# Optimization experiments

Measured on AMD Instinct MI355X. Metric: run time of the kernel, lower is better.

## Reference

```python
import jax, jax.numpy as jnp
import numpy as np

E, H, I, T = 8, 1024, 2816, 512
E4M3_MAX = 448.0  # torch.finfo(float8_e4m3fn).max


def _quantize_to_fp8(w):
    # per-tensor dynamic scaling, identical to quantize_to_fp8 in the source
    amax = jnp.max(jnp.abs(w))
    scale = jnp.maximum(amax / E4M3_MAX, 1e-12)
    fp8 = (w / scale).astype(jnp.float8_e4m3fn)
    return fp8, scale.reshape(1).astype(jnp.float32)


def setup_inputs() -> dict:
    key = jax.random.key(0)
    k1, k2, k3, k4 = jax.random.split(key, 4)
    x = jax.random.normal(k1, (T, H), jnp.float32)
    expert_idx = jax.random.randint(k2, (T,), 0, E)
    # learned 3D expert params (stored compressed as fp8 + per-tensor scale)
    w_gu = jax.random.normal(k3, (E, 2 * I, H), jnp.float32) * 0.02
    w_d = jax.random.normal(k4, (E, H, I), jnp.float32) * 0.02
    w_gu_fp8, w_gu_scale = _quantize_to_fp8(w_gu)
    w_d_fp8, w_d_scale = _quantize_to_fp8(w_d)
    return {
        "x": x,
        "expert_idx": expert_idx,
        "w_gu_fp8": w_gu_fp8,
        "w_gu_scale": w_gu_scale,
        "w_d_fp8": w_d_fp8,
        "w_d_scale": w_d_scale,
    }


def reference(x, expert_idx, w_gu_fp8, w_gu_scale, w_d_fp8, w_d_scale):
    # materialize(): dequantize fp8 -> high precision (fp8.to(dtype) * scale)
    w_gu = w_gu_fp8.astype(jnp.float32) * w_gu_scale  # [E, 2I, H]
    w_d = w_d_fp8.astype(jnp.float32) * w_d_scale     # [E, H, I]
    # inner experts forward: SwiGLU MLP per expert, top-1 routed tokens
    gu = jnp.einsum('th,efh->tef', x, w_gu)            # [T, E, 2I]
    gate, up = jnp.split(gu, 2, axis=-1)               # [T, E, I] each
    h = jax.nn.silu(gate) * up                          # [T, E, I]
    y = jnp.einsum('tei,ehi->teh', h, w_d)              # [T, E, H]
    out = y[jnp.arange(x.shape[0]), expert_idx]         # [T, H] select routed expert
    return out
```

## Files before the change

### kernel.cpp

```cpp
#include <hip/hip_runtime.h>
#include <hip/hip_bf16.h>
#include <stdint.h>

#define E_ 8
#define H_ 1024
#define I_ 2816
#define T_ 512

typedef __attribute__((ext_vector_type(4))) float f32x4;
typedef __attribute__((ext_vector_type(8))) short short8;

typedef __attribute__((address_space(1))) const unsigned GAS;
typedef __attribute__((address_space(3))) unsigned LAS;

__device__ __forceinline__ void dma16(const void* g, void* l) {
    __builtin_amdgcn_global_load_lds((GAS*)g, (LAS*)l, 16, 0, 0);
}
__device__ __forceinline__ unsigned short f2bf(float f) {
    return __builtin_bit_cast(unsigned short, __float2bfloat16(f));
}
__device__ __forceinline__ uint32_t pack_rne(float lo, float hi) {
    return (uint32_t)f2bf(lo) | ((uint32_t)f2bf(hi) << 16);
}
__device__ __forceinline__ uint32_t pack_trunc(float lo, float hi) {
    return (__builtin_bit_cast(uint32_t, hi) & 0xFFFF0000u) |
           (__builtin_bit_cast(uint32_t, lo) >> 16);
}

#define VM6() asm volatile("s_waitcnt vmcnt(6)" ::: "memory")
#define VM0() asm volatile("s_waitcnt vmcnt(0)" ::: "memory")

__global__ __launch_bounds__(256) void route_cvt(const float* __restrict__ x,
                                                 const int* __restrict__ idx,
                                                 int* __restrict__ counts,
                                                 int* __restrict__ bucket,
                                                 unsigned short* __restrict__ xg) {
    int tid = threadIdx.x;
    if (blockIdx.x == 0) {
        if (tid < E_) counts[tid] = 0;
        for (int i = tid; i < E_ * T_; i += 256) bucket[i] = 0;
        __syncthreads();
#pragma unroll
        for (int k = 0; k < 2; ++k) {
            int t = tid + k * 256;
            int e = idx[t];
            int pos = atomicAdd(counts + e, 1);
            bucket[e * T_ + pos] = t;
        }
    }
    int unit = blockIdx.x * 256 + tid;
    const float* xp = x + (size_t)unit * 8;
    float4 a = *(const float4*)xp, b = *(const float4*)(xp + 4);
    uint4 o = make_uint4(pack_rne(a.x, a.y), pack_rne(a.z, a.w),
                         pack_rne(b.x, b.y), pack_rne(b.z, b.w));
    *(uint4*)(xg + (size_t)unit * 8) = o;
}

__global__ __launch_bounds__(256) void gemm1(const unsigned short* __restrict__ xg,
                                             const float* __restrict__ wgu,
                                             const float* __restrict__ sgu_p,
                                             const int* __restrict__ counts,
                                             const int* __restrict__ bucket,
                                             __hip_bfloat16* __restrict__ hbuf) {
    int e = blockIdx.x >> 1, mt = blockIdx.x & 1;
    int cnt = counts[e];
    if (mt * 64 >= cnt) return;
    int f0 = blockIdx.y * 32;

    __shared__ __align__(16) char smem[72 * 1024 + 256];
    int* tok = (int*)(smem + 72 * 1024);
    int tid = threadIdx.x, w = tid >> 6, lane = tid & 63;
    int r16 = lane & 15, kg = lane >> 4;

    float sgu = sgu_p[0];
    asm volatile("" :: "v"(sgu));

    if (tid < 64) tok[tid] = bucket[e * T_ + mt * 64 + tid];
    __syncthreads();

    const char* xb = (const char*)xg;
    const char* srcA[2]; char* dstA[2];
#pragma unroll
    for (int i = 0; i < 2; ++i) {
        int U = (w * 2 + i) * 64 + lane;
        int row = U >> 3, sl = U & 7;
        srcA[i] = xb + (size_t)tok[row] * 2048 + (size_t)((sl ^ (row & 7)) * 16);
        dstA[i] = smem + (w * 2 + i) * 1024;
    }
    const char* wg_e = (const char*)(wgu + (size_t)e * 2 * (size_t)I_ * H_);
    const char* srcB[4]; char* dstB[4];
#pragma unroll
    for (int i = 0; i < 4; ++i) {
        int U = (w * 4 + i) * 64 + lane;
        int row = U >> 4, sl = U & 15;
        int wr = (row < 32) ? (f0 + row) : (I_ + f0 + row - 32);
        srcB[i] = wg_e + (size_t)wr * 4096 + (size_t)((sl ^ (row & 15)) * 16);
        dstB[i] = smem + 24 * 1024 + (w * 4 + i) * 1024;
    }

#define G1_ISSUE(s, buf)                                                     \
    do {                                                                     \
        _Pragma("unroll")                                                    \
        for (int i = 0; i < 2; ++i) dma16(srcA[i] + (size_t)(s) * 128, dstA[i] + (buf) * 8192);  \
        _Pragma("unroll")                                                    \
        for (int i = 0; i < 4; ++i) dma16(srcB[i] + (size_t)(s) * 256, dstB[i] + (buf) * 16384); \
    } while (0)

    G1_ISSUE(0, 0);
    G1_ISSUE(1, 1);

    f32x4 acc[4];
#pragma unroll
    for (int m = 0; m < 4; ++m) acc[m] = (f32x4){0, 0, 0, 0};

    for (int t = 0; t < 16; ++t) {
        VM6();
        __builtin_amdgcn_s_barrier();
        int tp = (t + 2 < 16) ? t + 2 : 15;
        G1_ISSUE(tp, (t + 2) % 3);
        const char* Ab = smem + (t % 3) * 8192;
        const char* Bb = smem + 24 * 1024 + (t % 3) * 16384;
#pragma unroll
        for (int kk = 0; kk < 2; ++kk) {
            int brow = w * 16 + r16;
            int bo = brow * 256 + kk * 128 + kg * 32;
            int sw = r16 << 4;
            float4 b0 = *(float4*)(Bb + (bo ^ sw));
            float4 b1 = *(float4*)(Bb + ((bo + 16) ^ sw));
            uint4 bu = make_uint4(pack_trunc(b0.x, b0.y), pack_trunc(b0.z, b0.w),
                                  pack_trunc(b1.x, b1.y), pack_trunc(b1.z, b1.w));
            short8 B = __builtin_bit_cast(short8, bu);
#pragma unroll
            for (int m = 0; m < 4; ++m) {
                int ar = m * 16 + r16;
                short8 A = *(short8*)(Ab + ((ar * 128 + kk * 64 + kg * 16) ^ ((ar & 7) << 4)));
                acc[m] = __builtin_amdgcn_mfma_f32_16x16x32_bf16(A, B, acc[m], 0, 0, 0);
            }
        }
    }
    VM0();
    __syncthreads();

    float* ex = (float*)smem;
    if (w >= 2) {
        float* dst = ex + (w - 2) * 1024;
#pragma unroll
        for (int m = 0; m < 4; ++m)
#pragma unroll
            for (int j = 0; j < 4; ++j)
                dst[(m * 16 + kg * 4 + j) * 16 + r16] = acc[m][j] * sgu;
    }
    __syncthreads();
    if (w < 2) {
        const float* src = ex + w * 1024;
#pragma unroll
        for (int m = 0; m < 4; ++m)
#pragma unroll
            for (int j = 0; j < 4; ++j) {
                int tr = m * 16 + kg * 4 + j;
                int pos = mt * 64 + tr;
                if (pos < cnt) {
                    float g = acc[m][j] * sgu;
                    float u = src[tr * 16 + r16];
                    float hv = (g / (1.f + __expf(-g))) * u;
                    hbuf[(size_t)tok[tr] * I_ + f0 + w * 16 + r16] = __float2bfloat16(hv);
                }
            }
    }
}

__global__ __launch_bounds__(256) void gemm2(const __hip_bfloat16* __restrict__ hbuf,
                                             const float* __restrict__ wd,
                                             const float* __restrict__ sd_p,
                                             const int* __restrict__ counts,
                                             const int* __restrict__ bucket,
                                             float* __restrict__ out) {
    int e = blockIdx.x >> 1, mt = blockIdx.x & 1;
    int cnt = counts[e];
    if (mt * 64 >= cnt) return;
    int h0 = blockIdx.y * 16;

    __shared__ __align__(16) char smem[72 * 1024 + 256];
    int* tok = (int*)(smem + 72 * 1024);
    int tid = threadIdx.x, w = tid >> 6, lane = tid & 63;
    int r16 = lane & 15, kg = lane >> 4;

    float sd = sd_p[0];
    asm volatile("" :: "v"(sd));

    if (tid < 64) tok[tid] = bucket[e * T_ + mt * 64 + tid];
    __syncthreads();

    const char* hb = (const char*)hbuf;
    const char* srcA[4]; char* dstA[4];
#pragma unroll
    for (int i = 0; i < 4; ++i) {
        int U = (w * 4 + i) * 64 + lane;
        int row = U >> 4, sl = U & 15;
        srcA[i] = hb + (size_t)tok[row] * (I_ * 2) + (size_t)((sl ^ (row & 15)) * 16);
        dstA[i] = smem + (w * 4 + i) * 1024;
    }
    const char* wd_e = (const char*)(wd + (size_t)e * (size_t)H_ * I_);
    const char* srcB[2]; char* dstB[2];
#pragma unroll
    for (int i = 0; i < 2; ++i) {
        int U = (w * 2 + i) * 64 + lane;
        int row = U >> 5, sl = U & 31;
        srcB[i] = wd_e + (size_t)(h0 + row) * ((size_t)I_ * 4) + (size_t)((sl ^ (row & 15)) * 16);
        dstB[i] = smem + 48 * 1024 + (w * 2 + i) * 1024;
    }

#define G2_ISSUE(s, buf)                                                     \
    do {                                                                     \
        _Pragma("unroll")                                                    \
        for (int i = 0; i < 4; ++i) dma16(srcA[i] + (size_t)(s) * 256, dstA[i] + (buf) * 16384); \
        _Pragma("unroll")                                                    \
        for (int i = 0; i < 2; ++i) dma16(srcB[i] + (size_t)(s) * 512, dstB[i] + (buf) * 8192);  \
    } while (0)

    G2_ISSUE(0, 0);
    G2_ISSUE(1, 1);

    f32x4 acc = (f32x4){0, 0, 0, 0};

    for (int t = 0; t < 22; ++t) {
        VM6();
        __builtin_amdgcn_s_barrier();
        int tp = (t + 2 < 22) ? t + 2 : 21;
        G2_ISSUE(tp, (t + 2) % 3);
        const char* Ab = smem + (t % 3) * 16384;
        const char* Bb = smem + 48 * 1024 + (t % 3) * 8192;
#pragma unroll
        for (int kk = 0; kk < 4; ++kk) {
            int bo = r16 * 512 + kk * 128 + kg * 32;
            int sw = r16 << 4;
            float4 b0 = *(float4*)(Bb + (bo ^ sw));
            float4 b1 = *(float4*)(Bb + ((bo + 16) ^ sw));
            uint4 bu = make_uint4(pack_trunc(b0.x, b0.y), pack_trunc(b0.z, b0.w),
                                  pack_trunc(b1.x, b1.y), pack_trunc(b1.z, b1.w));
            short8 B = __builtin_bit_cast(short8, bu);
            int ar = w * 16 + r16;
            short8 A = *(short8*)(Ab + ((ar * 256 + kk * 64 + kg * 16) ^ ((ar & 15) << 4)));
            acc = __builtin_amdgcn_mfma_f32_16x16x32_bf16(A, B, acc, 0, 0, 0);
        }
    }
    VM0();

#pragma unroll
    for (int j = 0; j < 4; ++j) {
        int tr = w * 16 + kg * 4 + j;
        int pos = mt * 64 + tr;
        if (pos < cnt)
            out[(size_t)tok[tr] * H_ + h0 + r16] = acc[j] * sd;
    }
}

extern "C" void kernel_launch(void* const* d_in, const int* in_sizes, int n_in,
                              void* d_out, int out_size, void* d_ws, size_t ws_size,
                              hipStream_t stream) {
    const float* x    = (const float*)d_in[0];
    const int*   eidx = (const int*)d_in[1];
    const float* wgu  = (const float*)d_in[2];
    const float* sgu  = (const float*)d_in[3];
    const float* wd   = (const float*)d_in[4];
    const float* sd   = (const float*)d_in[5];
    float* out = (float*)d_out;

    char* ws = (char*)d_ws;
    int* counts = (int*)ws;
    int* bucket = (int*)(ws + 1024);
    unsigned short* xg = (unsigned short*)(ws + 32768);
    __hip_bfloat16* hbuf = (__hip_bfloat16*)(ws + 1114112);

    route_cvt<<<256, 256, 0, stream>>>(x, eidx, counts, bucket, xg);
    gemm1<<<dim3(E_ * 2, I_ / 32), 256, 0, stream>>>(xg, wgu, sgu, counts, bucket, hbuf);
    gemm2<<<dim3(E_ * 2, H_ / 16), 256, 0, stream>>>(hbuf, wd, sd, counts, bucket, out);
}
```

Measured before the change: 121.7 us.

## Widen token tile to 128 rows so each expert's weights stream once

Both GEMMs now cover up to 128 routed tokens per block instead of 64. The per-step K slice is halved, so the three-stage LDS pipeline still fits and the loop runs more iterations. With about 64 tokens per expert on average, the old tiling made experts with more than 64 tokens read their fp32 weight slices twice, and the larger tile is meant to remove that duplicate traffic. gemm2 also doubles its output width to 32 columns using a 2x2 warp layout. The cost is wasted MFMA work on padded rows and more accumulator registers per thread.

After: 238.8 us. 1.96x slower.

```diff
diff --git a/kernel.cpp b/kernel.cpp
--- a/kernel.cpp
+++ b/kernel.cpp
@@ -28,6 +28,7 @@
 }
 
 #define VM6() asm volatile("s_waitcnt vmcnt(6)" ::: "memory")
+#define VM4() asm volatile("s_waitcnt vmcnt(4)" ::: "memory")
 #define VM0() asm volatile("s_waitcnt vmcnt(0)" ::: "memory")
 
 __global__ __launch_bounds__(256) void route_cvt(const float* __restrict__ x,
@@ -62,103 +63,92 @@
                                              const int* __restrict__ counts,
                                              const int* __restrict__ bucket,
                                              __hip_bfloat16* __restrict__ hbuf) {
-    int e = blockIdx.x >> 1, mt = blockIdx.x & 1;
+    int e = blockIdx.x >> 2, mt = blockIdx.x & 3;
     int cnt = counts[e];
-    if (mt * 64 >= cnt) return;
+    if (mt * 128 >= cnt) return;
     int f0 = blockIdx.y * 32;
 
-    __shared__ __align__(16) char smem[72 * 1024 + 256];
-    int* tok = (int*)(smem + 72 * 1024);
+    __shared__ __align__(16) char smem[48 * 1024 + 512];
+    int* tok = (int*)(smem + 48 * 1024);
     int tid = threadIdx.x, w = tid >> 6, lane = tid & 63;
     int r16 = lane & 15, kg = lane >> 4;
 
-    float sgu = sgu_p[0];
-    asm volatile("" :: "v"(sgu));
-
-    if (tid < 64) tok[tid] = bucket[e * T_ + mt * 64 + tid];
+    if (tid < 128) tok[tid] = bucket[e * T_ + mt * 128 + tid];
     __syncthreads();
 
     const char* xb = (const char*)xg;
     const char* srcA[2]; char* dstA[2];
 #pragma unroll
     for (int i = 0; i < 2; ++i) {
-        int U = (w * 2 + i) * 64 + lane;
-        int row = U >> 3, sl = U & 7;
-        srcA[i] = xb + (size_t)tok[row] * 2048 + (size_t)((sl ^ (row & 7)) * 16);
-        dstA[i] = smem + (w * 2 + i) * 1024;
-    }
-    const char* wg_e = (const char*)(wgu + (size_t)e * 2 * (size_t)I_ * H_);
-    const char* srcB[4]; char* dstB[4];
-#pragma unroll
-    for (int i = 0; i < 4; ++i) {
-        int U = (w * 4 + i) * 64 + lane;
-        int row = U >> 4, sl = U & 15;
+        int gi = w * 2 + i;
+        int row = gi * 16 + (lane >> 2), sl = lane & 3;
+        srcA[i] = xb + (size_t)tok[row] * 2048 + sl * 16;
+        dstA[i] = smem + gi * 1024;
+    }
+    const char* wg_e = (const char*)wgu + (size_t)e * (2 * (size_t)I_ * H_ * 4);
+    const char* srcB[2]; char* dstB[2];
+#pragma unroll
+    for (int i = 0; i < 2; ++i) {
+        int gi = w * 2 + i;
+        int row = gi * 8 + (lane >> 3), sl = lane & 7;
         int wr = (row < 32) ? (f0 + row) : (I_ + f0 + row - 32);
-        srcB[i] = wg_e + (size_t)wr * 4096 + (size_t)((sl ^ (row & 15)) * 16);
-        dstB[i] = smem + 24 * 1024 + (w * 4 + i) * 1024;
-    }
-
-#define G1_ISSUE(s, buf)                                                     \
-    do {                                                                     \
-        _Pragma("unroll")                                                    \
-        for (int i = 0; i < 2; ++i) dma16(srcA[i] + (size_t)(s) * 128, dstA[i] + (buf) * 8192);  \
-        _Pragma("unroll")                                                    \
-        for (int i = 0; i < 4; ++i) dma16(srcB[i] + (size_t)(s) * 256, dstB[i] + (buf) * 16384); \
-    } while (0)
-
-    G1_ISSUE(0, 0);
-    G1_ISSUE(1, 1);
-
-    f32x4 acc[4];
-#pragma unroll
-    for (int m = 0; m < 4; ++m) acc[m] = (f32x4){0, 0, 0, 0};
-
-    for (int t = 0; t < 16; ++t) {
-        VM6();
+        srcB[i] = wg_e + (size_t)wr * 4096 + ((sl ^ (row & 7)) * 16);
+        dstB[i] = smem + 24 * 1024 + gi * 1024;
+    }
+
+#define G1I(s, b) do {                                                               \
+    _Pragma("unroll")                                                                \
+    for (int i = 0; i < 2; ++i) dma16(srcA[i] + (size_t)(s) * 64,  dstA[i] + (b) * 8192); \
+    _Pragma("unroll")                                                                \
+    for (int i = 0; i < 2; ++i) dma16(srcB[i] + (size_t)(s) * 128, dstB[i] + (b) * 8192); } while (0)
+
+    G1I(0, 0);
+    G1I(1, 1);
+
+    f32x4 acc[8];
+#pragma unroll
+    for (int m = 0; m < 8; ++m) acc[m] = (f32x4){0, 0, 0, 0};
+
+    for (int t = 0; t < 32; ++t) {
+        if (t < 30) { VM4(); } else { VM0(); }
+        __builtin_amdgcn_sched_barrier(0);
         __builtin_amdgcn_s_barrier();
-        int tp = (t + 2 < 16) ? t + 2 : 15;
-        G1_ISSUE(tp, (t + 2) % 3);
+        if (t + 2 < 32) G1I(t + 2, (t + 2) % 3);
         const char* Ab = smem + (t % 3) * 8192;
-        const char* Bb = smem + 24 * 1024 + (t % 3) * 16384;
-#pragma unroll
-        for (int kk = 0; kk < 2; ++kk) {
-            int brow = w * 16 + r16;
-            int bo = brow * 256 + kk * 128 + kg * 32;
-            int sw = r16 << 4;
-            float4 b0 = *(float4*)(Bb + (bo ^ sw));
-            float4 b1 = *(float4*)(Bb + ((bo + 16) ^ sw));
-            uint4 bu = make_uint4(pack_trunc(b0.x, b0.y), pack_trunc(b0.z, b0.w),
-                                  pack_trunc(b1.x, b1.y), pack_trunc(b1.z, b1.w));
-            short8 B = __builtin_bit_cast(short8, bu);
-#pragma unroll
-            for (int m = 0; m < 4; ++m) {
-                int ar = m * 16 + r16;
-                short8 A = *(short8*)(Ab + ((ar * 128 + kk * 64 + kg * 16) ^ ((ar & 7) << 4)));
-                acc[m] = __builtin_amdgcn_mfma_f32_16x16x32_bf16(A, B, acc[m], 0, 0, 0);
-            }
-        }
-    }
-    VM0();
-    __syncthreads();
-
+        const char* Bb = smem + 24 * 1024 + (t % 3) * 8192;
+        int br = w * 16 + r16;
+        float4 b0 = *(const float4*)(Bb + br * 128 + (((2 * kg)     ^ (br & 7)) * 16));
+        float4 b1 = *(const float4*)(Bb + br * 128 + (((2 * kg + 1) ^ (br & 7)) * 16));
+        uint4 bu = make_uint4(pack_trunc(b0.x, b0.y), pack_trunc(b0.z, b0.w),
+                              pack_trunc(b1.x, b1.y), pack_trunc(b1.z, b1.w));
+        short8 B = __builtin_bit_cast(short8, bu);
+#pragma unroll
+        for (int m = 0; m < 8; ++m) {
+            short8 A = *(const short8*)(Ab + (m * 16 + r16) * 64 + kg * 16);
+            acc[m] = __builtin_amdgcn_mfma_f32_16x16x32_bf16(A, B, acc[m], 0, 0, 0);
+        }
+    }
+    __syncthreads();
+
+    float sgu = sgu_p[0];
     float* ex = (float*)smem;
     if (w >= 2) {
-        float* dst = ex + (w - 2) * 1024;
-#pragma unroll
-        for (int m = 0; m < 4; ++m)
+        float* dst = ex + (w - 2) * 2048;
+#pragma unroll
+        for (int m = 0; m < 8; ++m)
 #pragma unroll
             for (int j = 0; j < 4; ++j)
                 dst[(m * 16 + kg * 4 + j) * 16 + r16] = acc[m][j] * sgu;
     }
     __syncthreads();
     if (w < 2) {
-        const float* src = ex + w * 1024;
-#pragma unroll
-        for (int m = 0; m < 4; ++m)
+        const float* src = ex + w * 2048;
+#pragma unroll
+        for (int m = 0; m < 8; ++m)
 #pragma unroll
             for (int j = 0; j < 4; ++j) {
                 int tr = m * 16 + kg * 4 + j;
-                int pos = mt * 64 + tr;
+                int pos = mt * 128 + tr;
                 if (pos < cnt) {
                     float g = acc[m][j] * sgu;
                     float u = src[tr * 16 + r16];
@@ -175,84 +165,86 @@
                                              const int* __restrict__ counts,
                                              const int* __restrict__ bucket,
                                              float* __restrict__ out) {
-    int e = blockIdx.x >> 1, mt = blockIdx.x & 1;
+    int e = blockIdx.x >> 2, mt = blockIdx.x & 3;
     int cnt = counts[e];
-    if (mt * 64 >= cnt) return;
-    int h0 = blockIdx.y * 16;
-
-    __shared__ __align__(16) char smem[72 * 1024 + 256];
+    if (mt * 128 >= cnt) return;
+    int h0 = blockIdx.y * 32;
+
+    __shared__ __align__(16) char smem[72 * 1024 + 512];
     int* tok = (int*)(smem + 72 * 1024);
     int tid = threadIdx.x, w = tid >> 6, lane = tid & 63;
     int r16 = lane & 15, kg = lane >> 4;
-
-    float sd = sd_p[0];
-    asm volatile("" :: "v"(sd));
-
-    if (tid < 64) tok[tid] = bucket[e * T_ + mt * 64 + tid];
+    int mg = w >> 1, ng = w & 1;
+
+    if (tid < 128) tok[tid] = bucket[e * T_ + mt * 128 + tid];
     __syncthreads();
 
     const char* hb = (const char*)hbuf;
     const char* srcA[4]; char* dstA[4];
 #pragma unroll
     for (int i = 0; i < 4; ++i) {
-        int U = (w * 4 + i) * 64 + lane;
-        int row = U >> 4, sl = U & 15;
-        srcA[i] = hb + (size_t)tok[row] * (I_ * 2) + (size_t)((sl ^ (row & 15)) * 16);
-        dstA[i] = smem + (w * 4 + i) * 1024;
-    }
-    const char* wd_e = (const char*)(wd + (size_t)e * (size_t)H_ * I_);
+        int gi = w * 4 + i;
+        int row = gi * 8 + (lane >> 3), sl = lane & 7;
+        srcA[i] = hb + (size_t)tok[row] * 5632 + ((sl ^ (row & 7)) * 16);
+        dstA[i] = smem + gi * 1024;
+    }
+    const char* wd_e = (const char*)wd + (size_t)e * ((size_t)H_ * I_ * 4);
     const char* srcB[2]; char* dstB[2];
 #pragma unroll
     for (int i = 0; i < 2; ++i) {
-        int U = (w * 2 + i) * 64 + lane;
-        int row = U >> 5, sl = U & 31;
-        srcB[i] = wd_e + (size_t)(h0 + row) * ((size_t)I_ * 4) + (size_t)((sl ^ (row & 15)) * 16);
-        dstB[i] = smem + 48 * 1024 + (w * 2 + i) * 1024;
-    }
-
-#define G2_ISSUE(s, buf)                                                     \
-    do {                                                                     \
-        _Pragma("unroll")                                                    \
-        for (int i = 0; i < 4; ++i) dma16(srcA[i] + (size_t)(s) * 256, dstA[i] + (buf) * 16384); \
-        _Pragma("unroll")                                                    \
-        for (int i = 0; i < 2; ++i) dma16(srcB[i] + (size_t)(s) * 512, dstB[i] + (buf) * 8192);  \
-    } while (0)
-
-    G2_ISSUE(0, 0);
-    G2_ISSUE(1, 1);
-
-    f32x4 acc = (f32x4){0, 0, 0, 0};
-
-    for (int t = 0; t < 22; ++t) {
-        VM6();
+        int gi = w * 2 + i;
+        int row = gi * 4 + (lane >> 4), sl = lane & 15;
+        srcB[i] = wd_e + (size_t)(h0 + row) * 11264 + ((sl ^ (row & 15)) * 16);
+        dstB[i] = smem + 48 * 1024 + gi * 1024;
+    }
+
+#define G2I(s, b) do {                                                                \
+    _Pragma("unroll")                                                                 \
+    for (int i = 0; i < 4; ++i) dma16(srcA[i] + (size_t)(s) * 128, dstA[i] + (b) * 16384); \
+    _Pragma("unroll")                                                                 \
+    for (int i = 0; i < 2; ++i) dma16(srcB[i] + (size_t)(s) * 256, dstB[i] + (b) * 8192);  } while (0)
+
+    G2I(0, 0);
+    G2I(1, 1);
+
+    f32x4 acc[4];
+#pragma unroll
+    for (int m = 0; m < 4; ++m) acc[m] = (f32x4){0, 0, 0, 0};
+
+    for (int t = 0; t < 44; ++t) {
+        if (t < 42) { VM6(); } else { VM0(); }
+        __builtin_amdgcn_sched_barrier(0);
         __builtin_amdgcn_s_barrier();
-        int tp = (t + 2 < 22) ? t + 2 : 21;
-        G2_ISSUE(tp, (t + 2) % 3);
+        if (t + 2 < 44) G2I(t + 2, (t + 2) % 3);
         const char* Ab = smem + (t % 3) * 16384;
         const char* Bb = smem + 48 * 1024 + (t % 3) * 8192;
 #pragma unroll
-        for (int kk = 0; kk < 4; ++kk) {
-            int bo = r16 * 512 + kk * 128 + kg * 32;
-            int sw = r16 << 4;
-            float4 b0 = *(float4*)(Bb + (bo ^ sw));
-            float4 b1 = *(float4*)(Bb + ((bo + 16) ^ sw));
+        for (int kk = 0; kk < 2; ++kk) {
+            int brow = ng * 16 + r16;
+            float4 b0 = *(const float4*)(Bb + brow * 256 + (((kk * 8 + 2 * kg)     ^ (brow & 15)) * 16));
+            float4 b1 = *(const float4*)(Bb + brow * 256 + (((kk * 8 + 2 * kg + 1) ^ (brow & 15)) * 16));
             uint4 bu = make_uint4(pack_trunc(b0.x, b0.y), pack_trunc(b0.z, b0.w),
                                   pack_trunc(b1.x, b1.y), pack_trunc(b1.z, b1.w));
             short8 B = __builtin_bit_cast(short8, bu);
-            int ar = w * 16 + r16;
-            short8 A = *(short8*)(Ab + ((ar * 256 + kk * 64 + kg * 16) ^ ((ar & 15) << 4)));
-            acc = __builtin_amdgcn_mfma_f32_16x16x32_bf16(A, B, acc, 0, 0, 0);
-        }
-    }
-    VM0();
-
-#pragma unroll
-    for (int j = 0; j < 4; ++j) {
-        int tr = w * 16 + kg * 4 + j;
-        int pos = mt * 64 + tr;
-        if (pos < cnt)
-            out[(size_t)tok[tr] * H_ + h0 + r16] = acc[j] * sd;
-    }
+#pragma unroll
+            for (int m = 0; m < 4; ++m) {
+                int arow = mg * 64 + m * 16 + r16;
+                short8 A = *(const short8*)(Ab + arow * 128 + (((kk * 4 + kg) ^ (arow & 7)) * 16));
+                acc[m] = __builtin_amdgcn_mfma_f32_16x16x32_bf16(A, B, acc[m], 0, 0, 0);
+            }
+        }
+    }
+
+    float sd = sd_p[0];
+#pragma unroll
+    for (int m = 0; m < 4; ++m)
+#pragma unroll
+        for (int j = 0; j < 4; ++j) {
+            int tr = mg * 64 + m * 16 + kg * 4 + j;
+            int pos = mt * 128 + tr;
+            if (pos < cnt)
+                out[(size_t)tok[tr] * H_ + h0 + ng * 16 + r16] = acc[m][j] * sd;
+        }
 }
 
 extern "C" void kernel_launch(void* const* d_in, const int* in_sizes, int n_in,
@@ -273,6 +265,6 @@
     __hip_bfloat16* hbuf = (__hip_bfloat16*)(ws + 1114112);
 
     route_cvt<<<256, 256, 0, stream>>>(x, eidx, counts, bucket, xg);
-    gemm1<<<dim3(E_ * 2, I_ / 32), 256, 0, stream>>>(xg, wgu, sgu, counts, bucket, hbuf);
-    gemm2<<<dim3(E_ * 2, H_ / 16), 256, 0, stream>>>(hbuf, wd, sd, counts, bucket, out);
-}
+    gemm1<<<dim3(E_ * 4, I_ / 32), 256, 0, stream>>>(xg, wgu, sgu, counts, bucket, hbuf);
+    gemm2<<<dim3(E_ * 4, H_ / 32), 256, 0, stream>>>(hbuf, wd, sd, counts, bucket, out);
+}
```

## Restructure gemm1 to stream weights from registers with 128-token tiles

Applied to the files above, without the earlier changes.

gemm1 now handles all 128 token slots of an expert per block (one M tile instead of two) and 64 feature columns, so each weight row is read once per expert rather than twice. Weights are loaded directly into registers with a two-deep software prefetch instead of DMA into LDS. Activations are gathered into LDS in four K-chunks. Gate and up accumulators live in the same wave, which removes the LDS exchange in the SwiGLU epilogue. The risks are the hard assumption of at most 128 tokens per expert, higher register pressure from 16 accumulators, and extra barriers around each activation reload.

After: 116.2 us. -4.5%, faster.

```diff
diff --git a/kernel.cpp b/kernel.cpp
--- a/kernel.cpp
+++ b/kernel.cpp
@@ -62,111 +62,95 @@
                                              const int* __restrict__ counts,
                                              const int* __restrict__ bucket,
                                              __hip_bfloat16* __restrict__ hbuf) {
-    int e = blockIdx.x >> 1, mt = blockIdx.x & 1;
+    int e = blockIdx.x;
     int cnt = counts[e];
-    if (mt * 64 >= cnt) return;
-    int f0 = blockIdx.y * 32;
-
-    __shared__ __align__(16) char smem[72 * 1024 + 256];
-    int* tok = (int*)(smem + 72 * 1024);
+    int f0 = blockIdx.y * 64;
+
+    __shared__ __align__(16) char sA[64 * 1024 + 512];
+    int* tok = (int*)(sA + 64 * 1024);
     int tid = threadIdx.x, w = tid >> 6, lane = tid & 63;
     int r16 = lane & 15, kg = lane >> 4;
 
+    const float* gp = wgu + (size_t)e * 2 * (size_t)I_ * H_ +
+                      (size_t)(f0 + w * 16 + r16) * H_ + kg * 8;
+    const float* up = gp + (size_t)I_ * H_;
+
+#define LOADW(NX, GA, GB, UA, UB)                                   \
+    do {                                                            \
+        const float* p_ = gp + (size_t)(NX) * 32;                   \
+        GA = *(const float4*)p_; GB = *(const float4*)(p_ + 4);     \
+        const float* q_ = up + (size_t)(NX) * 32;                   \
+        UA = *(const float4*)q_; UB = *(const float4*)(q_ + 4);     \
+    } while (0)
+
+    float4 g0a, g0b, u0a, u0b, g1a, g1b, u1a, u1b;
+    LOADW(0, g0a, g0b, u0a, u0b);
+    LOADW(1, g1a, g1b, u1a, u1b);
+
+    if (tid < 128) tok[tid] = bucket[e * T_ + tid];
+    __syncthreads();
+
+    f32x4 accg[8], accu[8];
+#pragma unroll
+    for (int m = 0; m < 8; ++m) { accg[m] = (f32x4){0,0,0,0}; accu[m] = (f32x4){0,0,0,0}; }
+
+#define CSTEP(J, GA, GB, UA, UB)                                                        \
+    do {                                                                                \
+        uint4 bg_ = make_uint4(pack_trunc((GA).x,(GA).y), pack_trunc((GA).z,(GA).w),    \
+                               pack_trunc((GB).x,(GB).y), pack_trunc((GB).z,(GB).w));   \
+        uint4 bu_ = make_uint4(pack_trunc((UA).x,(UA).y), pack_trunc((UA).z,(UA).w),    \
+                               pack_trunc((UB).x,(UB).y), pack_trunc((UB).z,(UB).w));   \
+        short8 Bg_ = __builtin_bit_cast(short8, bg_);                                   \
+        short8 Bu_ = __builtin_bit_cast(short8, bu_);                                   \
+        const char* ab_ = sA + (((J) * 4 + kg) << 11);                                  \
+        _Pragma("unroll")                                                               \
+        for (int m_ = 0; m_ < 8; ++m_) {                                                \
+            short8 A_ = *(const short8*)(ab_ + ((m_ * 16 + r16) << 4));                 \
+            accg[m_] = __builtin_amdgcn_mfma_f32_16x16x32_bf16(A_, Bg_, accg[m_],0,0,0);\
+            accu[m_] = __builtin_amdgcn_mfma_f32_16x16x32_bf16(A_, Bu_, accu[m_],0,0,0);\
+        }                                                                               \
+    } while (0)
+
+    for (int q = 0; q < 4; ++q) {
+        __syncthreads();
+#pragma unroll
+        for (int i = 0; i < 16; ++i) {
+            int u = tid + i * 256;
+            int s = u >> 7, t_ = u & 127;
+            uint4 v = *(const uint4*)(xg + (size_t)tok[t_] * H_ + q * 256 + s * 8);
+            *(uint4*)(sA + s * 2048 + t_ * 16) = v;
+        }
+        __syncthreads();
+#pragma unroll
+        for (int j = 0; j < 8; j += 2) {
+            CSTEP(j, g0a, g0b, u0a, u0b);
+            {
+                int nx = q * 8 + j + 2; if (nx > 31) nx = 31;
+                LOADW(nx, g0a, g0b, u0a, u0b);
+            }
+            CSTEP(j + 1, g1a, g1b, u1a, u1b);
+            {
+                int nx = q * 8 + j + 3; if (nx > 31) nx = 31;
+                LOADW(nx, g1a, g1b, u1a, u1b);
+            }
+        }
+    }
+
     float sgu = sgu_p[0];
-    asm volatile("" :: "v"(sgu));
-
-    if (tid < 64) tok[tid] = bucket[e * T_ + mt * 64 + tid];
-    __syncthreads();
-
-    const char* xb = (const char*)xg;
-    const char* srcA[2]; char* dstA[2];
-#pragma unroll
-    for (int i = 0; i < 2; ++i) {
-        int U = (w * 2 + i) * 64 + lane;
-        int row = U >> 3, sl = U & 7;
-        srcA[i] = xb + (size_t)tok[row] * 2048 + (size_t)((sl ^ (row & 7)) * 16);
-        dstA[i] = smem + (w * 2 + i) * 1024;
-    }
-    const char* wg_e = (const char*)(wgu + (size_t)e * 2 * (size_t)I_ * H_);
-    const char* srcB[4]; char* dstB[4];
-#pragma unroll
-    for (int i = 0; i < 4; ++i) {
-        int U = (w * 4 + i) * 64 + lane;
-        int row = U >> 4, sl = U & 15;
-        int wr = (row < 32) ? (f0 + row) : (I_ + f0 + row - 32);
-        srcB[i] = wg_e + (size_t)wr * 4096 + (size_t)((sl ^ (row & 15)) * 16);
-        dstB[i] = smem + 24 * 1024 + (w * 4 + i) * 1024;
-    }
-
-#define G1_ISSUE(s, buf)                                                     \
-    do {                                                                     \
-        _Pragma("unroll")                                                    \
-        for (int i = 0; i < 2; ++i) dma16(srcA[i] + (size_t)(s) * 128, dstA[i] + (buf) * 8192);  \
-        _Pragma("unroll")                                                    \
-        for (int i = 0; i < 4; ++i) dma16(srcB[i] + (size_t)(s) * 256, dstB[i] + (buf) * 16384); \
-    } while (0)
-
-    G1_ISSUE(0, 0);
-    G1_ISSUE(1, 1);
-
-    f32x4 acc[4];
-#pragma unroll
-    for (int m = 0; m < 4; ++m) acc[m] = (f32x4){0, 0, 0, 0};
-
-    for (int t = 0; t < 16; ++t) {
-        VM6();
-        __builtin_amdgcn_s_barrier();
-        int tp = (t + 2 < 16) ? t + 2 : 15;
-        G1_ISSUE(tp, (t + 2) % 3);
-        const char* Ab = smem + (t % 3) * 8192;
-        const char* Bb = smem + 24 * 1024 + (t % 3) * 16384;
-#pragma unroll
-        for (int kk = 0; kk < 2; ++kk) {
-            int brow = w * 16 + r16;
-            int bo = brow * 256 + kk * 128 + kg * 32;
-            int sw = r16 << 4;
-            float4 b0 = *(float4*)(Bb + (bo ^ sw));
-            float4 b1 = *(float4*)(Bb + ((bo + 16) ^ sw));
-            uint4 bu = make_uint4(pack_trunc(b0.x, b0.y), pack_trunc(b0.z, b0.w),
-                                  pack_trunc(b1.x, b1.y), pack_trunc(b1.z, b1.w));
-            short8 B = __builtin_bit_cast(short8, bu);
-#pragma unroll
-            for (int m = 0; m < 4; ++m) {
-                int ar = m * 16 + r16;
-                short8 A = *(short8*)(Ab + ((ar * 128 + kk * 64 + kg * 16) ^ ((ar & 7) << 4)));
-                acc[m] = __builtin_amdgcn_mfma_f32_16x16x32_bf16(A, B, acc[m], 0, 0, 0);
+#pragma unroll
+    for (int m = 0; m < 8; ++m)
+#pragma unroll
+        for (int j = 0; j < 4; ++j) {
+            int tr = m * 16 + kg * 4 + j;
+            if (tr < cnt) {
+                float g = accg[m][j] * sgu;
+                float u = accu[m][j] * sgu;
+                float hv = (g / (1.f + __expf(-g))) * u;
+                hbuf[(size_t)tok[tr] * I_ + f0 + w * 16 + r16] = __float2bfloat16(hv);
             }
         }
-    }
-    VM0();
-    __syncthreads();
-
-    float* ex = (float*)smem;
-    if (w >= 2) {
-        float* dst = ex + (w - 2) * 1024;
-#pragma unroll
-        for (int m = 0; m < 4; ++m)
-#pragma unroll
-            for (int j = 0; j < 4; ++j)
-                dst[(m * 16 + kg * 4 + j) * 16 + r16] = acc[m][j] * sgu;
-    }
-    __syncthreads();
-    if (w < 2) {
-        const float* src = ex + w * 1024;
-#pragma unroll
-        for (int m = 0; m < 4; ++m)
-#pragma unroll
-            for (int j = 0; j < 4; ++j) {
-                int tr = m * 16 + kg * 4 + j;
-                int pos = mt * 64 + tr;
-                if (pos < cnt) {
-                    float g = acc[m][j] * sgu;
-                    float u = src[tr * 16 + r16];
-                    float hv = (g / (1.f + __expf(-g))) * u;
-                    hbuf[(size_t)tok[tr] * I_ + f0 + w * 16 + r16] = __float2bfloat16(hv);
-                }
-            }
-    }
+#undef CSTEP
+#undef LOADW
 }
 
 __global__ __launch_bounds__(256) void gemm2(const __hip_bfloat16* __restrict__ hbuf,
@@ -253,6 +237,7 @@
         if (pos < cnt)
             out[(size_t)tok[tr] * H_ + h0 + r16] = acc[j] * sd;
     }
+#undef G2_ISSUE
 }
 
 extern "C" void kernel_launch(void* const* d_in, const int* in_sizes, int n_in,
@@ -273,6 +258,6 @@
     __hip_bfloat16* hbuf = (__hip_bfloat16*)(ws + 1114112);
 
     route_cvt<<<256, 256, 0, stream>>>(x, eidx, counts, bucket, xg);
-    gemm1<<<dim3(E_ * 2, I_ / 32), 256, 0, stream>>>(xg, wgu, sgu, counts, bucket, hbuf);
+    gemm1<<<dim3(E_, I_ / 64), 256, 0, stream>>>(xg, wgu, sgu, counts, bucket, hbuf);
     gemm2<<<dim3(E_ * 2, H_ / 16), 256, 0, stream>>>(hbuf, wd, sd, counts, bucket, out);
 }
```

## Restructure gemm1 to one block per expert with fused gate/up accumulators

Applied to the files above, without the earlier changes.

gemm1 now covers all of an expert's tokens (up to 128) in a single block over a narrower 16-feature slice. Each gate/up weight tile is therefore streamed from memory once per expert, not once per 64-token M tile. Each warp keeps separate gate and up accumulators, so the LDS exchange and the extra barriers in the SwiGLU epilogue go away. The pipeline is reworked to double-buffer activations and triple-buffer weights. The cost is more activation traffic per block and wasted MFMA work on empty token rows. It also assumes no expert receives more than 128 tokens.

Result: faster. 113.8 us (-6.5%).

```diff
diff --git a/kernel.cpp b/kernel.cpp
--- a/kernel.cpp
+++ b/kernel.cpp
@@ -27,6 +27,7 @@
            (__builtin_bit_cast(uint32_t, lo) >> 16);
 }
 
+#define VM2() asm volatile("s_waitcnt vmcnt(2)" ::: "memory")
 #define VM6() asm volatile("s_waitcnt vmcnt(6)" ::: "memory")
 #define VM0() asm volatile("s_waitcnt vmcnt(0)" ::: "memory")
 
@@ -62,111 +63,100 @@
                                              const int* __restrict__ counts,
                                              const int* __restrict__ bucket,
                                              __hip_bfloat16* __restrict__ hbuf) {
-    int e = blockIdx.x >> 1, mt = blockIdx.x & 1;
+    int e = blockIdx.x;
+    int f0 = blockIdx.y * 16;
     int cnt = counts[e];
-    if (mt * 64 >= cnt) return;
-    int f0 = blockIdx.y * 32;
-
-    __shared__ __align__(16) char smem[72 * 1024 + 256];
-    int* tok = (int*)(smem + 72 * 1024);
+
+    __shared__ __align__(16) char smem[56 * 1024 + 512];
+    int* tok = (int*)(smem + 56 * 1024);
     int tid = threadIdx.x, w = tid >> 6, lane = tid & 63;
     int r16 = lane & 15, kg = lane >> 4;
 
-    float sgu = sgu_p[0];
-    asm volatile("" :: "v"(sgu));
-
-    if (tid < 64) tok[tid] = bucket[e * T_ + mt * 64 + tid];
+    if (tid < 128) tok[tid] = bucket[e * T_ + tid];
     __syncthreads();
 
     const char* xb = (const char*)xg;
-    const char* srcA[2]; char* dstA[2];
+    const char* srcA[4]; char* dstA[4];
+#pragma unroll
+    for (int i = 0; i < 4; ++i) {
+        int U = (w * 4 + i) * 64 + lane;
+        int t_ = U >> 3, sl = U & 7;
+        srcA[i] = xb + (size_t)tok[t_] * 2048 + ((sl ^ (t_ & 7)) * 16);
+        dstA[i] = smem + (w * 4 + i) * 1024;
+    }
+    const char* wbase = (const char*)wgu + (size_t)e * 2 * (size_t)I_ * H_ * 4;
+    const char* srcB[2]; char* dstB[2];
 #pragma unroll
     for (int i = 0; i < 2; ++i) {
         int U = (w * 2 + i) * 64 + lane;
-        int row = U >> 3, sl = U & 7;
-        srcA[i] = xb + (size_t)tok[row] * 2048 + (size_t)((sl ^ (row & 7)) * 16);
-        dstA[i] = smem + (w * 2 + i) * 1024;
-    }
-    const char* wg_e = (const char*)(wgu + (size_t)e * 2 * (size_t)I_ * H_);
-    const char* srcB[4]; char* dstB[4];
-#pragma unroll
-    for (int i = 0; i < 4; ++i) {
-        int U = (w * 4 + i) * 64 + lane;
         int row = U >> 4, sl = U & 15;
-        int wr = (row < 32) ? (f0 + row) : (I_ + f0 + row - 32);
-        srcB[i] = wg_e + (size_t)wr * 4096 + (size_t)((sl ^ (row & 15)) * 16);
-        dstB[i] = smem + 24 * 1024 + (w * 4 + i) * 1024;
-    }
-
-#define G1_ISSUE(s, buf)                                                     \
-    do {                                                                     \
-        _Pragma("unroll")                                                    \
-        for (int i = 0; i < 2; ++i) dma16(srcA[i] + (size_t)(s) * 128, dstA[i] + (buf) * 8192);  \
-        _Pragma("unroll")                                                    \
-        for (int i = 0; i < 4; ++i) dma16(srcB[i] + (size_t)(s) * 256, dstB[i] + (buf) * 16384); \
-    } while (0)
-
-    G1_ISSUE(0, 0);
-    G1_ISSUE(1, 1);
-
-    f32x4 acc[4];
-#pragma unroll
-    for (int m = 0; m < 4; ++m) acc[m] = (f32x4){0, 0, 0, 0};
+        int wr = (row < 16) ? (f0 + row) : (I_ + f0 + row - 16);
+        srcB[i] = wbase + (size_t)wr * 4096 + ((sl ^ (row & 15)) * 16);
+        dstB[i] = smem + 32 * 1024 + (w * 2 + i) * 1024;
+    }
+
+#pragma unroll
+    for (int i = 0; i < 2; ++i) dma16(srcB[i], dstB[i]);
+#pragma unroll
+    for (int i = 0; i < 4; ++i) dma16(srcA[i], dstA[i]);
+#pragma unroll
+    for (int i = 0; i < 2; ++i) dma16(srcB[i] + 256, dstB[i] + 8192);
+
+    f32x4 accg[2], accu[2];
+#pragma unroll
+    for (int m = 0; m < 2; ++m) { accg[m] = (f32x4){0,0,0,0}; accu[m] = (f32x4){0,0,0,0}; }
 
     for (int t = 0; t < 16; ++t) {
-        VM6();
+        VM2();
+        __builtin_amdgcn_sched_barrier(0);
         __builtin_amdgcn_s_barrier();
-        int tp = (t + 2 < 16) ? t + 2 : 15;
-        G1_ISSUE(tp, (t + 2) % 3);
-        const char* Ab = smem + (t % 3) * 8192;
-        const char* Bb = smem + 24 * 1024 + (t % 3) * 16384;
+        int sa = (t + 1 < 16) ? t + 1 : 15;
+        int sb = (t + 2 < 16) ? t + 2 : 15;
+#pragma unroll
+        for (int i = 0; i < 4; ++i)
+            dma16(srcA[i] + (size_t)sa * 128, dstA[i] + ((t + 1) & 1) * 16384);
+#pragma unroll
+        for (int i = 0; i < 2; ++i)
+            dma16(srcB[i] + (size_t)sb * 256, dstB[i] + ((t + 2) % 3) * 8192);
+
+        const char* Ab = smem + (t & 1) * 16384;
+        const char* Bb = smem + 32 * 1024 + (t % 3) * 8192;
 #pragma unroll
         for (int kk = 0; kk < 2; ++kk) {
-            int brow = w * 16 + r16;
-            int bo = brow * 256 + kk * 128 + kg * 32;
-            int sw = r16 << 4;
-            float4 b0 = *(float4*)(Bb + (bo ^ sw));
-            float4 b1 = *(float4*)(Bb + ((bo + 16) ^ sw));
-            uint4 bu = make_uint4(pack_trunc(b0.x, b0.y), pack_trunc(b0.z, b0.w),
-                                  pack_trunc(b1.x, b1.y), pack_trunc(b1.z, b1.w));
-            short8 B = __builtin_bit_cast(short8, bu);
-#pragma unroll
-            for (int m = 0; m < 4; ++m) {
-                int ar = m * 16 + r16;
-                short8 A = *(short8*)(Ab + ((ar * 128 + kk * 64 + kg * 16) ^ ((ar & 7) << 4)));
-                acc[m] = __builtin_amdgcn_mfma_f32_16x16x32_bf16(A, B, acc[m], 0, 0, 0);
+            int s0 = kk * 8 + kg * 2;
+            float4 g0 = *(const float4*)(Bb + r16 * 256 + ((s0 ^ r16) * 16));
+            float4 g1 = *(const float4*)(Bb + r16 * 256 + (((s0 + 1) ^ r16) * 16));
+            float4 u0 = *(const float4*)(Bb + (16 + r16) * 256 + ((s0 ^ r16) * 16));
+            float4 u1 = *(const float4*)(Bb + (16 + r16) * 256 + (((s0 + 1) ^ r16) * 16));
+            uint4 bg = make_uint4(pack_trunc(g0.x, g0.y), pack_trunc(g0.z, g0.w),
+                                  pack_trunc(g1.x, g1.y), pack_trunc(g1.z, g1.w));
+            uint4 bu = make_uint4(pack_trunc(u0.x, u0.y), pack_trunc(u0.z, u0.w),
+                                  pack_trunc(u1.x, u1.y), pack_trunc(u1.z, u1.w));
+            short8 Bg = __builtin_bit_cast(short8, bg);
+            short8 Bu = __builtin_bit_cast(short8, bu);
+#pragma unroll
+            for (int m = 0; m < 2; ++m) {
+                int tr = w * 32 + m * 16 + r16;
+                short8 A = *(const short8*)(Ab + tr * 128 + (((kk * 4 + kg) ^ (tr & 7)) * 16));
+                accg[m] = __builtin_amdgcn_mfma_f32_16x16x32_bf16(A, Bg, accg[m], 0, 0, 0);
+                accu[m] = __builtin_amdgcn_mfma_f32_16x16x32_bf16(A, Bu, accu[m], 0, 0, 0);
             }
         }
     }
-    VM0();
-    __syncthreads();
-
-    float* ex = (float*)smem;
-    if (w >= 2) {
-        float* dst = ex + (w - 2) * 1024;
-#pragma unroll
-        for (int m = 0; m < 4; ++m)
-#pragma unroll
-            for (int j = 0; j < 4; ++j)
-                dst[(m * 16 + kg * 4 + j) * 16 + r16] = acc[m][j] * sgu;
-    }
-    __syncthreads();
-    if (w < 2) {
-        const float* src = ex + w * 1024;
-#pragma unroll
-        for (int m = 0; m < 4; ++m)
-#pragma unroll
-            for (int j = 0; j < 4; ++j) {
-                int tr = m * 16 + kg * 4 + j;
-                int pos = mt * 64 + tr;
-                if (pos < cnt) {
-                    float g = acc[m][j] * sgu;
-                    float u = src[tr * 16 + r16];
-                    float hv = (g / (1.f + __expf(-g))) * u;
-                    hbuf[(size_t)tok[tr] * I_ + f0 + w * 16 + r16] = __float2bfloat16(hv);
-                }
+
+    float sgu = sgu_p[0];
+#pragma unroll
+    for (int m = 0; m < 2; ++m)
+#pragma unroll
+        for (int j = 0; j < 4; ++j) {
+            int tk = w * 32 + m * 16 + kg * 4 + j;
+            if (tk < cnt) {
+                float g = accg[m][j] * sgu;
+                float u = accu[m][j] * sgu;
+                float hv = (g / (1.f + __expf(-g))) * u;
+                hbuf[(size_t)tok[tk] * I_ + f0 + r16] = __float2bfloat16(hv);
             }
-    }
+        }
 }
 
 __global__ __launch_bounds__(256) void gemm2(const __hip_bfloat16* __restrict__ hbuf,
@@ -253,6 +243,7 @@
         if (pos < cnt)
             out[(size_t)tok[tr] * H_ + h0 + r16] = acc[j] * sd;
     }
+#undef G2_ISSUE
 }
 
 extern "C" void kernel_launch(void* const* d_in, const int* in_sizes, int n_in,
@@ -273,6 +264,6 @@
     __hip_bfloat16* hbuf = (__hip_bfloat16*)(ws + 1114112);
 
     route_cvt<<<256, 256, 0, stream>>>(x, eidx, counts, bucket, xg);
-    gemm1<<<dim3(E_ * 2, I_ / 32), 256, 0, stream>>>(xg, wgu, sgu, counts, bucket, hbuf);
+    gemm1<<<dim3(E_, I_ / 16), 256, 0, stream>>>(xg, wgu, sgu, counts, bucket, hbuf);
     gemm2<<<dim3(E_ * 2, H_ / 16), 256, 0, stream>>>(hbuf, wd, sd, counts, bucket, out);
 }
```
